# Kernel optimization log

Measured on AMD Instinct MI355X. Metric: run time of the kernel, lower is better.

The kernel has to match this reference:

```python
import jax, jax.numpy as jnp
import numpy as np

B, D, H, Z, E = 65536, 128, 256, 128, 16  # batch, input, hidden, hyper, embedding


def setup_inputs() -> dict:
    key = jax.random.key(0)
    ks = jax.random.split(key, 20)
    s = 0.02  # small weight scale for numerical sanity
    return {
        "x": jax.random.normal(ks[0], (B, D), jnp.float32),
        "h0": jax.random.normal(ks[1], (B, H), jnp.float32),
        "c0": jax.random.normal(ks[2], (B, H), jnp.float32),
        "hhat0": jax.random.normal(ks[3], (B, Z), jnp.float32),
        "chat0": jax.random.normal(ks[4], (B, Z), jnp.float32),
        "hweight": jax.random.normal(ks[5], (Z + H + D, 4 * Z), jnp.float32) * s,
        "hbias": jnp.zeros((4 * Z,), jnp.float32),
        "zw_h": jax.random.normal(ks[6], (Z, 4 * E), jnp.float32) * s,
        "zw_x": jax.random.normal(ks[7], (Z, 4 * E), jnp.float32) * s,
        "zw_b": jax.random.normal(ks[8], (Z, 4 * E), jnp.float32) * 0.01,
        "zb_h": jnp.ones((4 * E,), jnp.float32),
        "zb_x": jnp.ones((4 * E,), jnp.float32),
        "dw_h": jnp.full((4, E, H), 0.1 / E, jnp.float32),  # [i,g,f,o] stacked
        "dw_x": jnp.full((4, E, H), 0.1 / E, jnp.float32),
        "dw_b": jax.random.normal(ks[9], (4, E, H), jnp.float32) * s,
        "weight": jax.random.normal(ks[10], (H + D, 4 * H), jnp.float32) * s,
        "bias": jnp.zeros((4 * H,), jnp.float32),
    }


def reference(x, h0, c0, hhat0, chat0, hweight, hbias, zw_h, zw_x, zw_b,
              zb_h, zb_x, dw_h, dw_x, dw_b, weight, bias):
    sig, tanh = jax.nn.sigmoid, jnp.tanh
    b = x.shape[0]
    # hyper LSTM cell
    gh = jnp.concatenate([hhat0, h0, x], axis=1) @ hweight + hbias  # [B, 4Z]
    i_h, g_h, f_h, o_h = jnp.split(gh, 4, axis=1)
    chat1 = sig(f_h) * chat0 + sig(i_h) * tanh(g_h)
    hhat1 = sig(o_h) * tanh(chat1)
    # embedding projections z (chunk order i,g,f,o -> reshape to [B,4,E])
    z_h = (hhat1 @ zw_h + zb_h).reshape(b, 4, E)
    z_x = (hhat1 @ zw_x + zb_x).reshape(b, 4, E)
    z_b = (hhat1 @ zw_b).reshape(b, 4, E)
    # d scaling vectors, [B,4,H] -> [B,4H]
    d_yh = jnp.einsum('bke,keh->bkh', z_h, dw_h).reshape(b, 4 * H)
    d_yx = jnp.einsum('bke,keh->bkh', z_x, dw_x).reshape(b, 4 * H)
    d_yb = jnp.einsum('bke,keh->bkh', z_b, dw_b).reshape(b, 4 * H)
    # main LSTM gates, hyper-modulated
    g = jnp.concatenate([h0, x], axis=1) @ weight * d_yh * d_yx + d_yb + bias
    i_g, g_g, f_g, o_g = jnp.split(g, 4, axis=1)
    c1 = sig(f_g) * c0 + sig(i_g) * tanh(g_g)
    h1 = sig(o_g) * tanh(c1)
    return (h1, c1, hhat1, chat1)
```

## Files before the change

kernel.cpp:

```cpp
#include <hip/hip_runtime.h>


typedef unsigned short u16;
typedef __attribute__((ext_vector_type(8))) short bf16x8;
typedef __attribute__((ext_vector_type(4))) float f32x4;

#define BATCH 65536

__device__ __forceinline__ u16 f2b(float f) {
  unsigned u = __float_as_uint(f);
  u += 0x7fffu + ((u >> 16) & 1u);
  return (u16)(u >> 16);
}
__device__ __forceinline__ unsigned pk2(float a, float b) {
  return (unsigned)f2b(a) | ((unsigned)f2b(b) << 16);
}
__device__ __forceinline__ float upk_lo(unsigned u) { return __uint_as_float(u << 16); }
__device__ __forceinline__ float upk_hi(unsigned u) { return __uint_as_float(u & 0xffff0000u); }
__device__ __forceinline__ float sigf(float x) { return 1.0f / (1.0f + __expf(-x)); }
__device__ __forceinline__ float tanhfast(float x) {
  float xc = fminf(fmaxf(x, -15.f), 15.f);
  float e = __expf(2.f * xc);
  return (e - 1.f) / (e + 1.f);
}
__device__ __forceinline__ int swz(int r, int c) { return r * 64 + (c ^ ((r & 7) << 3)); }

#define VM_BAR(N) do { \
  asm volatile("s_waitcnt vmcnt(" #N ")" ::: "memory"); \
  __builtin_amdgcn_s_barrier(); \
  __builtin_amdgcn_sched_barrier(0); } while (0)

__device__ __forceinline__ void gl_lds16(const u16* g, u16* l) {
  __builtin_amdgcn_global_load_lds(
      (const __attribute__((address_space(1))) void*)g,
      (__attribute__((address_space(3))) void*)l, 16, 0, 0);
}
__device__ __forceinline__ void stageA(const u16* base, int ldk, u16* lA, int t) {
  const int r = t >> 3, q = t & 7, wid = t >> 6;
  const int qs = (q ^ (r & 7)) << 3;
  gl_lds16(base + (size_t)r * ldk + qs, lA + wid * 512);
  gl_lds16(base + (size_t)(r + 32) * ldk + qs, lA + 2048 + wid * 512);
}

__global__ __launch_bounds__(256) void hlstm_pre(
    const float* __restrict__ hhat0, const float* __restrict__ h0,
    const float* __restrict__ x, u16* __restrict__ abuf,
    const float* __restrict__ hweight, const float* __restrict__ hbias,
    const float* __restrict__ zw_h, const float* __restrict__ zw_x, const float* __restrict__ zw_b,
    const float* __restrict__ zb_h, const float* __restrict__ zb_x,
    const float* __restrict__ dw_h, const float* __restrict__ dw_x, const float* __restrict__ dw_b,
    const float* __restrict__ weight, const float* __restrict__ bias,
    u16* __restrict__ hw_fr, float* __restrict__ hbias_r,
    u16* __restrict__ w_fr,  float* __restrict__ bias_r,
    u16* __restrict__ whp_fr, u16* __restrict__ wxp_fr, u16* __restrict__ wbp_fr,
    float* __restrict__ bhp_r, float* __restrict__ bxp_r)
{
  if (blockIdx.x < 4096) {
    const size_t stride = (size_t)4096 * 256;
    for (size_t i = (size_t)blockIdx.x * 256 + threadIdx.x;
         i < (size_t)BATCH * 64; i += stride) {
      const size_t b = i >> 6; const int c = (int)(i & 63);
      const float* src;
      if (c < 16)      src = hhat0 + b * 128 + c * 8;
      else if (c < 48) src = h0 + b * 256 + (size_t)(c - 16) * 8;
      else             src = x + b * 128 + (size_t)(c - 48) * 8;
      float4 v0 = ((const float4*)src)[0];
      float4 v1 = ((const float4*)src)[1];
      alignas(16) u16 o[8] = {f2b(v0.x), f2b(v0.y), f2b(v0.z), f2b(v0.w),
                              f2b(v1.x), f2b(v1.y), f2b(v1.z), f2b(v1.w)};
      *(uint4*)(abuf + i * 8) = *(const uint4*)o;
    }
    return;
  }
  const int tid = (blockIdx.x - 4096) * 256 + threadIdx.x;
  const int nt  = 512 * 256;

  for (int i = tid; i < 16 * 16384; i += nt) {
    int tile = i >> 14, r = i & 16383;
    int wc = r >> 12, h = (r >> 11) & 1, g = (r >> 9) & 3;
    int lane = (r >> 3) & 63, j = r & 7;
    int hb = tile >> 3, s = tile & 7;
    int k = s * 64 + h * 32 + (lane >> 4) * 8 + j;
    int col = g * 128 + hb * 64 + wc * 16 + (lane & 15);
    hw_fr[i] = f2b(hweight[k * 512 + col]);
  }
  for (int i = tid; i < 24 * 16384; i += nt) {
    int tile = i >> 14, r = i & 16383;
    int wc = r >> 12, h = (r >> 11) & 1, g = (r >> 9) & 3;
    int lane = (r >> 3) & 63, j = r & 7;
    int hb = tile / 6, s = tile % 6;
    int k = s * 64 + h * 32 + (lane >> 4) * 8 + j;
    int col = g * 256 + hb * 64 + wc * 16 + (lane & 15);
    w_fr[i] = f2b(weight[k * 1024 + col]);
  }
  for (int i = tid; i < 3 * 8 * 16384; i += nt) {
    int mat = i / (8 * 16384), rem = i % (8 * 16384);
    int tile = rem >> 14, r = rem & 16383;
    int wc = r >> 12, h = (r >> 11) & 1, g = (r >> 9) & 3;
    int lane = (r >> 3) & 63, j = r & 7;
    int hb = tile >> 1, s = tile & 1;
    int k = s * 64 + h * 32 + (lane >> 4) * 8 + j;
    int colh = hb * 64 + wc * 16 + (lane & 15);
    const float* zw = (mat == 0) ? zw_h : (mat == 1) ? zw_x : zw_b;
    const float* dw = (mat == 0) ? dw_h : (mat == 1) ? dw_x : dw_b;
    float sv = 0.f;
#pragma unroll
    for (int e = 0; e < 16; ++e)
      sv += zw[k * 64 + g * 16 + e] * dw[g * 4096 + e * 256 + colh];
    u16* dst = (mat == 0) ? whp_fr : (mat == 1) ? wxp_fr : wbp_fr;
    dst[rem] = f2b(sv);
  }
  for (int i = tid; i < 1024; i += nt) {
    int hb = i >> 8, g = (i >> 6) & 3, hh = i & 63;
    int h = hb * 64 + hh;
    float sh = 0.f, sx = 0.f;
#pragma unroll
    for (int e = 0; e < 16; ++e) {
      sh += zb_h[g * 16 + e] * dw_h[g * 4096 + e * 256 + h];
      sx += zb_x[g * 16 + e] * dw_x[g * 4096 + e * 256 + h];
    }
    bhp_r[i] = sh; bxp_r[i] = sx;
    bias_r[i] = bias[g * 256 + h];
  }
  for (int i = tid; i < 512; i += nt) {
    int gate = (i >> 6) & 3, hb = i >> 8, hh = i & 63;
    hbias_r[i] = hbias[gate * 128 + hb * 64 + hh];
  }
}

__global__ __launch_bounds__(256, 3) void hlstm_k1(
    const u16* __restrict__ abuf, const float* __restrict__ chat0,
    const u16* __restrict__ hw_fr, const float* __restrict__ hbias_r,
    float* __restrict__ d_out, u16* __restrict__ hbuf)
{
  __shared__ alignas(16) u16 lA[3][64 * 64];
  const int f = blockIdx.x;
  const int xcd = f & 7, s2 = f >> 3;
  const int rb = xcd * 128 + (s2 >> 1), hb = s2 & 1;
  const int t = threadIdx.x;
  const int lane = t & 63, wc = t >> 6;
  const int lr = lane & 15, kg = lane >> 4;

  f32x4 acc[4][4];
  const f32x4 zzero = {0.f, 0.f, 0.f, 0.f};
#pragma unroll
  for (int mf = 0; mf < 4; ++mf)
#pragma unroll
    for (int g = 0; g < 4; ++g) acc[mf][g] = zzero;

  const u16* arow = abuf + (size_t)rb * 64 * 512;

  bf16x8 breg[8];
  auto loadB = [&](const u16* bt) {
#pragma unroll
    for (int h = 0; h < 2; ++h)
#pragma unroll
      for (int g = 0; g < 4; ++g)
        breg[h * 4 + g] = *(const bf16x8*)&bt[((wc * 2 + h) * 4 + g) * 512 + lane * 8];
  };
  auto sweep = [&](f32x4 (&ac)[4][4], const u16* cA) {
#pragma unroll
    for (int h = 0; h < 2; ++h)
#pragma unroll
      for (int mf = 0; mf < 4; ++mf) {
        bf16x8 afr = *(const bf16x8*)&cA[swz(mf * 16 + lr, h * 32 + kg * 8)];
#pragma unroll
        for (int g = 0; g < 4; ++g)
          ac[mf][g] = __builtin_amdgcn_mfma_f32_16x16x32_bf16(afr, breg[h * 4 + g], ac[mf][g], 0, 0, 0);
      }
  };

  stageA(arow + 0 * 64, 512, lA[0], t);
  stageA(arow + 1 * 64, 512, lA[1], t);
  loadB(hw_fr + (size_t)(hb * 8 + 0) * 16384);
  VM_BAR(8);

#pragma unroll
  for (int ks = 0; ks < 8; ++ks) {
    if (ks < 6) stageA(arow + (ks + 2) * 64, 512, lA[(ks + 2) % 3], t);
    sweep(acc, lA[ks % 3]);
    if (ks < 7) loadB(hw_fr + (size_t)(hb * 8 + ks + 1) * 16384);
    if (ks < 6)       VM_BAR(10);
    else if (ks == 6) VM_BAR(8);
  }

  float hb4[4];
#pragma unroll
  for (int g = 0; g < 4; ++g) hb4[g] = hbias_r[hb * 256 + g * 64 + wc * 16 + lr];
  const int zc = hb * 64 + wc * 16 + lr;
  float* out_hh = d_out + (size_t)BATCH * 512;
  float* out_ch = d_out + (size_t)BATCH * 640;
#pragma unroll
  for (int mf = 0; mf < 4; ++mf)
#pragma unroll
    for (int r = 0; r < 4; ++r) {
      const int row = rb * 64 + mf * 16 + kg * 4 + r;
      const float gi = acc[mf][0][r] + hb4[0];
      const float gg = acc[mf][1][r] + hb4[1];
      const float gf = acc[mf][2][r] + hb4[2];
      const float go = acc[mf][3][r] + hb4[3];
      const float c0v = chat0[(size_t)row * 128 + zc];
      const float c1v = sigf(gf) * c0v + sigf(gi) * tanhfast(gg);
      const float h1v = sigf(go) * tanhfast(c1v);
      out_hh[(size_t)row * 128 + zc] = h1v;
      out_ch[(size_t)row * 128 + zc] = c1v;
      hbuf[(size_t)row * 128 + zc] = f2b(h1v);
    }
}

__global__ __launch_bounds__(256, 2) void hlstm_k2(
    const u16* __restrict__ abuf, const u16* __restrict__ hbuf,
    const float* __restrict__ c0,
    const u16* __restrict__ w_fr, const float* __restrict__ bias_r,
    const u16* __restrict__ whp_fr, const u16* __restrict__ wxp_fr, const u16* __restrict__ wbp_fr,
    const float* __restrict__ bhp_r, const float* __restrict__ bxp_r,
    float* __restrict__ d_out)
{
  __shared__ alignas(16) u16 lA[3][64 * 64];
  const int f = blockIdx.x;
  const int xcd = f & 7, s4 = f >> 3;
  const int rb = xcd * 128 + (s4 >> 2), hb = s4 & 3;
  const int t = threadIdx.x;
  const int lane = t & 63, wc = t >> 6;
  const int lr = lane & 15, kg = lane >> 4;

  const u16* amain = abuf + (size_t)rb * 64 * 512 + 128;
  const u16* ahyp  = hbuf + (size_t)rb * 64 * 128;

  auto aptr = [&](int s) -> const u16* {
    if (s >= 4 && s < 10) return amain + (s - 4) * 64;
    return ahyp + (s & 1) * 64;
  };
  auto aldk = [&](int s) -> int { return (s >= 4 && s < 10) ? 512 : 128; };
  auto bptr = [&](int s) -> const u16* {
    if (s < 2)  return whp_fr + (size_t)(hb * 2 + s) * 16384;
    if (s < 4)  return wxp_fr + (size_t)(hb * 2 + s - 2) * 16384;
    if (s < 10) return w_fr  + (size_t)(hb * 6 + s - 4) * 16384;
    return wbp_fr + (size_t)(hb * 2 + s - 10) * 16384;
  };

  f32x4 acc[4][4];
  const f32x4 zzero = {0.f, 0.f, 0.f, 0.f};
#pragma unroll
  for (int mf = 0; mf < 4; ++mf)
#pragma unroll
    for (int g = 0; g < 4; ++g) acc[mf][g] = zzero;

  unsigned dsc[4][4][2];

  bf16x8 breg[8];
  auto loadB = [&](const u16* bt) {
#pragma unroll
    for (int h = 0; h < 2; ++h)
#pragma unroll
      for (int g = 0; g < 4; ++g)
        breg[h * 4 + g] = *(const bf16x8*)&bt[((wc * 2 + h) * 4 + g) * 512 + lane * 8];
  };
  auto sweep = [&](f32x4 (&ac)[4][4], const u16* cA) {
#pragma unroll
    for (int h = 0; h < 2; ++h)
#pragma unroll
      for (int mf = 0; mf < 4; ++mf) {
        bf16x8 afr = *(const bf16x8*)&cA[swz(mf * 16 + lr, h * 32 + kg * 8)];
#pragma unroll
        for (int g = 0; g < 4; ++g)
          ac[mf][g] = __builtin_amdgcn_mfma_f32_16x16x32_bf16(afr, breg[h * 4 + g], ac[mf][g], 0, 0, 0);
      }
  };

  stageA(aptr(0), aldk(0), lA[0], t);
  stageA(aptr(1), aldk(1), lA[1], t);
  loadB(bptr(0));
  VM_BAR(8);

#pragma unroll
  for (int s = 0; s < 12; ++s) {
    if (s < 10) stageA(aptr(s + 2), aldk(s + 2), lA[(s + 2) % 3], t);
    if (s == 2 || s == 4) {
#pragma unroll
      for (int mf = 0; mf < 4; ++mf)
#pragma unroll
        for (int g = 0; g < 4; ++g) acc[mf][g] = zzero;
    }
    sweep(acc, lA[s % 3]);
    if (s < 11) loadB(bptr(s + 1));
    if (s == 1) {
      float bh4[4];
#pragma unroll
      for (int g = 0; g < 4; ++g) bh4[g] = bhp_r[hb * 256 + g * 64 + wc * 16 + lr];
#pragma unroll
      for (int mf = 0; mf < 4; ++mf)
#pragma unroll
        for (int g = 0; g < 4; ++g) {
          dsc[mf][g][0] = pk2(acc[mf][g][0] + bh4[g], acc[mf][g][1] + bh4[g]);
          dsc[mf][g][1] = pk2(acc[mf][g][2] + bh4[g], acc[mf][g][3] + bh4[g]);
        }
    } else if (s == 3) {
      float bx4[4];
#pragma unroll
      for (int g = 0; g < 4; ++g) bx4[g] = bxp_r[hb * 256 + g * 64 + wc * 16 + lr];
#pragma unroll
      for (int mf = 0; mf < 4; ++mf)
#pragma unroll
        for (int g = 0; g < 4; ++g) {
          float d0 = upk_lo(dsc[mf][g][0]) * (acc[mf][g][0] + bx4[g]);
          float d1 = upk_hi(dsc[mf][g][0]) * (acc[mf][g][1] + bx4[g]);
          float d2 = upk_lo(dsc[mf][g][1]) * (acc[mf][g][2] + bx4[g]);
          float d3 = upk_hi(dsc[mf][g][1]) * (acc[mf][g][3] + bx4[g]);
          dsc[mf][g][0] = pk2(d0, d1);
          dsc[mf][g][1] = pk2(d2, d3);
        }
    } else if (s == 9) {
#pragma unroll
      for (int mf = 0; mf < 4; ++mf)
#pragma unroll
        for (int g = 0; g < 4; ++g) {
          acc[mf][g][0] *= upk_lo(dsc[mf][g][0]);
          acc[mf][g][1] *= upk_hi(dsc[mf][g][0]);
          acc[mf][g][2] *= upk_lo(dsc[mf][g][1]);
          acc[mf][g][3] *= upk_hi(dsc[mf][g][1]);
        }
    }
    if (s < 10)       VM_BAR(10);
    else if (s == 10) VM_BAR(8);
  }

  const int hcol = hb * 64 + wc * 16 + lr;
  float b4[4];
#pragma unroll
  for (int g = 0; g < 4; ++g) b4[g] = bias_r[hb * 256 + g * 64 + wc * 16 + lr];
  float* out_c1 = d_out + (size_t)BATCH * 256;
#pragma unroll
  for (int mf = 0; mf < 4; ++mf)
#pragma unroll
    for (int r = 0; r < 4; ++r) {
      const int row = rb * 64 + mf * 16 + kg * 4 + r;
      const float gi = acc[mf][0][r] + b4[0];
      const float gg = acc[mf][1][r] + b4[1];
      const float gf = acc[mf][2][r] + b4[2];
      const float go = acc[mf][3][r] + b4[3];
      const float c0v = c0[(size_t)row * 256 + hcol];
      const float c1v = sigf(gf) * c0v + sigf(gi) * tanhfast(gg);
      const float h1v = sigf(go) * tanhfast(c1v);
      d_out[(size_t)row * 256 + hcol]  = h1v;
      out_c1[(size_t)row * 256 + hcol] = c1v;
    }
}

extern "C" void kernel_launch(void* const* d_in, const int* in_sizes, int n_in,
                              void* d_out, int out_size, void* d_ws, size_t ws_size,
                              hipStream_t stream)
{
  (void)in_sizes; (void)n_in; (void)out_size; (void)ws_size;
  const float* x       = (const float*)d_in[0];
  const float* h0      = (const float*)d_in[1];
  const float* c0      = (const float*)d_in[2];
  const float* hhat0   = (const float*)d_in[3];
  const float* chat0   = (const float*)d_in[4];
  const float* hweight = (const float*)d_in[5];
  const float* hbias   = (const float*)d_in[6];
  const float* zw_h    = (const float*)d_in[7];
  const float* zw_x    = (const float*)d_in[8];
  const float* zw_b    = (const float*)d_in[9];
  const float* zb_h    = (const float*)d_in[10];
  const float* zb_x    = (const float*)d_in[11];
  const float* dw_h    = (const float*)d_in[12];
  const float* dw_x    = (const float*)d_in[13];
  const float* dw_b    = (const float*)d_in[14];
  const float* weight  = (const float*)d_in[15];
  const float* bias    = (const float*)d_in[16];

  char* wsb = (char*)d_ws;
  u16*   abuf    = (u16*)(wsb + 0);
  u16*   hbuf    = (u16*)(wsb + 67108864);
  u16*   hw_fr   = (u16*)(wsb + 83886080);
  u16*   w_fr    = (u16*)(wsb + 84410368);
  u16*   whp_fr  = (u16*)(wsb + 85196800);
  u16*   wxp_fr  = (u16*)(wsb + 85458944);
  u16*   wbp_fr  = (u16*)(wsb + 85721088);
  float* hbias_r = (float*)(wsb + 85983232);
  float* bias_r  = (float*)(wsb + 85985280);
  float* bhp_r   = (float*)(wsb + 85989376);
  float* bxp_r   = (float*)(wsb + 85993472);

  hlstm_pre<<<dim3(4608), dim3(256), 0, stream>>>(
      hhat0, h0, x, abuf,
      hweight, hbias, zw_h, zw_x, zw_b, zb_h, zb_x, dw_h, dw_x, dw_b, weight, bias,
      hw_fr, hbias_r, w_fr, bias_r, whp_fr, wxp_fr, wbp_fr, bhp_r, bxp_r);

  hlstm_k1<<<dim3(2048), dim3(256), 0, stream>>>(
      abuf, chat0, hw_fr, hbias_r, (float*)d_out, hbuf);

  hlstm_k2<<<dim3(4096), dim3(256), 0, stream>>>(
      abuf, hbuf, c0, w_fr, bias_r, whp_fr, wxp_fr, wbp_fr, bhp_r, bxp_r, (float*)d_out);
}
```

Baseline: 273.6 us.

## Pre-pack activations in MFMA fragment order and load A directly to registers

The pre-pass now writes the bf16 activation matrix in MFMA fragment order, so each lane's 16-byte A fragment is contiguous. Both GEMM kernels drop the LDS triple-buffer staging with global_load_lds and barriers, and instead double-buffer A and B fragments in registers by K-half. The aim is to remove the LDS round trip and block-wide synchronisation. The trade-off is that each of the four waves now reads the same A tile from global/L2 separately, which multiplies A traffic, and it raises register pressure.

New measurement: 391.3 us. 43.0% more time.

```diff
diff --git a/kernel.cpp b/kernel.cpp
--- a/kernel.cpp
+++ b/kernel.cpp
@@ -23,28 +23,10 @@
   float e = __expf(2.f * xc);
   return (e - 1.f) / (e + 1.f);
 }
-__device__ __forceinline__ int swz(int r, int c) { return r * 64 + (c ^ ((r & 7) << 3)); }
-
-#define VM_BAR(N) do { \
-  asm volatile("s_waitcnt vmcnt(" #N ")" ::: "memory"); \
-  __builtin_amdgcn_s_barrier(); \
-  __builtin_amdgcn_sched_barrier(0); } while (0)
-
-__device__ __forceinline__ void gl_lds16(const u16* g, u16* l) {
-  __builtin_amdgcn_global_load_lds(
-      (const __attribute__((address_space(1))) void*)g,
-      (__attribute__((address_space(3))) void*)l, 16, 0, 0);
-}
-__device__ __forceinline__ void stageA(const u16* base, int ldk, u16* lA, int t) {
-  const int r = t >> 3, q = t & 7, wid = t >> 6;
-  const int qs = (q ^ (r & 7)) << 3;
-  gl_lds16(base + (size_t)r * ldk + qs, lA + wid * 512);
-  gl_lds16(base + (size_t)(r + 32) * ldk + qs, lA + 2048 + wid * 512);
-}
 
 __global__ __launch_bounds__(256) void hlstm_pre(
     const float* __restrict__ hhat0, const float* __restrict__ h0,
-    const float* __restrict__ x, u16* __restrict__ abuf,
+    const float* __restrict__ x, u16* __restrict__ abuf_fr,
     const float* __restrict__ hweight, const float* __restrict__ hbias,
     const float* __restrict__ zw_h, const float* __restrict__ zw_x, const float* __restrict__ zw_b,
     const float* __restrict__ zb_h, const float* __restrict__ zb_x,
@@ -58,17 +40,23 @@
   if (blockIdx.x < 4096) {
     const size_t stride = (size_t)4096 * 256;
     for (size_t i = (size_t)blockIdx.x * 256 + threadIdx.x;
-         i < (size_t)BATCH * 64; i += stride) {
-      const size_t b = i >> 6; const int c = (int)(i & 63);
+         i < (size_t)4194304; i += stride) {
+      const int lane = (int)(i & 63);
+      const int h    = (int)((i >> 6) & 1);
+      const int mf   = (int)((i >> 7) & 3);
+      const int kc   = (int)((i >> 9) & 7);
+      const int rb   = (int)(i >> 12);
+      const int row = rb * 64 + mf * 16 + (lane & 15);
+      const int col = kc * 64 + h * 32 + (lane >> 4) * 8;
       const float* src;
-      if (c < 16)      src = hhat0 + b * 128 + c * 8;
-      else if (c < 48) src = h0 + b * 256 + (size_t)(c - 16) * 8;
-      else             src = x + b * 128 + (size_t)(c - 48) * 8;
+      if (col < 128)      src = hhat0 + (size_t)row * 128 + col;
+      else if (col < 384) src = h0 + (size_t)row * 256 + (col - 128);
+      else                src = x + (size_t)row * 128 + (col - 384);
       float4 v0 = ((const float4*)src)[0];
       float4 v1 = ((const float4*)src)[1];
       alignas(16) u16 o[8] = {f2b(v0.x), f2b(v0.y), f2b(v0.z), f2b(v0.w),
                               f2b(v1.x), f2b(v1.y), f2b(v1.z), f2b(v1.w)};
-      *(uint4*)(abuf + i * 8) = *(const uint4*)o;
+      *(uint4*)(abuf_fr + i * 8) = *(const uint4*)o;
     }
     return;
   }
@@ -129,11 +117,10 @@
 }
 
 __global__ __launch_bounds__(256, 3) void hlstm_k1(
-    const u16* __restrict__ abuf, const float* __restrict__ chat0,
+    const u16* __restrict__ abuf_fr, const float* __restrict__ chat0,
     const u16* __restrict__ hw_fr, const float* __restrict__ hbias_r,
     float* __restrict__ d_out, u16* __restrict__ hbuf)
 {
-  __shared__ alignas(16) u16 lA[3][64 * 64];
   const int f = blockIdx.x;
   const int xcd = f & 7, s2 = f >> 3;
   const int rb = xcd * 128 + (s2 >> 1), hb = s2 & 1;
@@ -148,40 +135,34 @@
 #pragma unroll
     for (int g = 0; g < 4; ++g) acc[mf][g] = zzero;
 
-  const u16* arow = abuf + (size_t)rb * 64 * 512;
-
-  bf16x8 breg[8];
-  auto loadB = [&](const u16* bt) {
-#pragma unroll
-    for (int h = 0; h < 2; ++h)
+  bf16x8 A0[4], A1[4], B0[4], B1[4];
+  auto loadA = [&](bf16x8 (&Ar)[4], int kc, int h) {
+#pragma unroll
+    for (int mf = 0; mf < 4; ++mf)
+      Ar[mf] = *(const bf16x8*)&abuf_fr[((((size_t)rb * 8 + kc) * 4 + mf) * 2 + h) * 512 + lane * 8];
+  };
+  auto loadBh = [&](bf16x8 (&Br)[4], const u16* bt, int h) {
+#pragma unroll
+    for (int g = 0; g < 4; ++g)
+      Br[g] = *(const bf16x8*)&bt[((wc * 2 + h) * 4 + g) * 512 + lane * 8];
+  };
+  auto half = [&](const bf16x8 (&Ar)[4], const bf16x8 (&Br)[4]) {
+#pragma unroll
+    for (int mf = 0; mf < 4; ++mf)
 #pragma unroll
       for (int g = 0; g < 4; ++g)
-        breg[h * 4 + g] = *(const bf16x8*)&bt[((wc * 2 + h) * 4 + g) * 512 + lane * 8];
-  };
-  auto sweep = [&](f32x4 (&ac)[4][4], const u16* cA) {
-#pragma unroll
-    for (int h = 0; h < 2; ++h)
-#pragma unroll
-      for (int mf = 0; mf < 4; ++mf) {
-        bf16x8 afr = *(const bf16x8*)&cA[swz(mf * 16 + lr, h * 32 + kg * 8)];
-#pragma unroll
-        for (int g = 0; g < 4; ++g)
-          ac[mf][g] = __builtin_amdgcn_mfma_f32_16x16x32_bf16(afr, breg[h * 4 + g], ac[mf][g], 0, 0, 0);
-      }
-  };
-
-  stageA(arow + 0 * 64, 512, lA[0], t);
-  stageA(arow + 1 * 64, 512, lA[1], t);
-  loadB(hw_fr + (size_t)(hb * 8 + 0) * 16384);
-  VM_BAR(8);
+        acc[mf][g] = __builtin_amdgcn_mfma_f32_16x16x32_bf16(Ar[mf], Br[g], acc[mf][g], 0, 0, 0);
+  };
+
+  loadA(A0, 0, 0); loadBh(B0, hw_fr + (size_t)(hb * 8) * 16384, 0);
+  loadA(A1, 0, 1); loadBh(B1, hw_fr + (size_t)(hb * 8) * 16384, 1);
 
 #pragma unroll
   for (int ks = 0; ks < 8; ++ks) {
-    if (ks < 6) stageA(arow + (ks + 2) * 64, 512, lA[(ks + 2) % 3], t);
-    sweep(acc, lA[ks % 3]);
-    if (ks < 7) loadB(hw_fr + (size_t)(hb * 8 + ks + 1) * 16384);
-    if (ks < 6)       VM_BAR(10);
-    else if (ks == 6) VM_BAR(8);
+    half(A0, B0);
+    if (ks < 7) { loadA(A0, ks + 1, 0); loadBh(B0, hw_fr + (size_t)(hb * 8 + ks + 1) * 16384, 0); }
+    half(A1, B1);
+    if (ks < 7) { loadA(A1, ks + 1, 1); loadBh(B1, hw_fr + (size_t)(hb * 8 + ks + 1) * 16384, 1); }
   }
 
   float hb4[4];
@@ -209,14 +190,13 @@
 }
 
 __global__ __launch_bounds__(256, 2) void hlstm_k2(
-    const u16* __restrict__ abuf, const u16* __restrict__ hbuf,
+    const u16* __restrict__ abuf_fr, const u16* __restrict__ hbuf,
     const float* __restrict__ c0,
     const u16* __restrict__ w_fr, const float* __restrict__ bias_r,
     const u16* __restrict__ whp_fr, const u16* __restrict__ wxp_fr, const u16* __restrict__ wbp_fr,
     const float* __restrict__ bhp_r, const float* __restrict__ bxp_r,
     float* __restrict__ d_out)
 {
-  __shared__ alignas(16) u16 lA[3][64 * 64];
   const int f = blockIdx.x;
   const int xcd = f & 7, s4 = f >> 3;
   const int rb = xcd * 128 + (s4 >> 2), hb = s4 & 3;
@@ -224,14 +204,6 @@
   const int lane = t & 63, wc = t >> 6;
   const int lr = lane & 15, kg = lane >> 4;
 
-  const u16* amain = abuf + (size_t)rb * 64 * 512 + 128;
-  const u16* ahyp  = hbuf + (size_t)rb * 64 * 128;
-
-  auto aptr = [&](int s) -> const u16* {
-    if (s >= 4 && s < 10) return amain + (s - 4) * 64;
-    return ahyp + (s & 1) * 64;
-  };
-  auto aldk = [&](int s) -> int { return (s >= 4 && s < 10) ? 512 : 128; };
   auto bptr = [&](int s) -> const u16* {
     if (s < 2)  return whp_fr + (size_t)(hb * 2 + s) * 16384;
     if (s < 4)  return wxp_fr + (size_t)(hb * 2 + s - 2) * 16384;
@@ -248,42 +220,49 @@
 
   unsigned dsc[4][4][2];
 
-  bf16x8 breg[8];
-  auto loadB = [&](const u16* bt) {
-#pragma unroll
-    for (int h = 0; h < 2; ++h)
+  bf16x8 A0[4], A1[4], B0[4], B1[4];
+  auto loadA = [&](bf16x8 (&Ar)[4], int s, int h) {
+    if (s >= 4 && s < 10) {
+      const int kc = s - 2;
+#pragma unroll
+      for (int mf = 0; mf < 4; ++mf)
+        Ar[mf] = *(const bf16x8*)&abuf_fr[((((size_t)rb * 8 + kc) * 4 + mf) * 2 + h) * 512 + lane * 8];
+    } else {
+      const int c = s & 1;
+#pragma unroll
+      for (int mf = 0; mf < 4; ++mf)
+        Ar[mf] = *(const bf16x8*)&hbuf[(size_t)(rb * 64 + mf * 16 + lr) * 128 + c * 64 + h * 32 + kg * 8];
+    }
+  };
+  auto loadBh = [&](bf16x8 (&Br)[4], const u16* bt, int h) {
+#pragma unroll
+    for (int g = 0; g < 4; ++g)
+      Br[g] = *(const bf16x8*)&bt[((wc * 2 + h) * 4 + g) * 512 + lane * 8];
+  };
+  auto half = [&](const bf16x8 (&Ar)[4], const bf16x8 (&Br)[4]) {
+#pragma unroll
+    for (int mf = 0; mf < 4; ++mf)
 #pragma unroll
       for (int g = 0; g < 4; ++g)
-        breg[h * 4 + g] = *(const bf16x8*)&bt[((wc * 2 + h) * 4 + g) * 512 + lane * 8];
-  };
-  auto sweep = [&](f32x4 (&ac)[4][4], const u16* cA) {
-#pragma unroll
-    for (int h = 0; h < 2; ++h)
-#pragma unroll
-      for (int mf = 0; mf < 4; ++mf) {
-        bf16x8 afr = *(const bf16x8*)&cA[swz(mf * 16 + lr, h * 32 + kg * 8)];
-#pragma unroll
-        for (int g = 0; g < 4; ++g)
-          ac[mf][g] = __builtin_amdgcn_mfma_f32_16x16x32_bf16(afr, breg[h * 4 + g], ac[mf][g], 0, 0, 0);
-      }
-  };
-
-  stageA(aptr(0), aldk(0), lA[0], t);
-  stageA(aptr(1), aldk(1), lA[1], t);
-  loadB(bptr(0));
-  VM_BAR(8);
+        acc[mf][g] = __builtin_amdgcn_mfma_f32_16x16x32_bf16(Ar[mf], Br[g], acc[mf][g], 0, 0, 0);
+  };
+
+  loadA(A0, 0, 0); loadBh(B0, bptr(0), 0);
+  loadA(A1, 0, 1); loadBh(B1, bptr(0), 1);
 
 #pragma unroll
   for (int s = 0; s < 12; ++s) {
-    if (s < 10) stageA(aptr(s + 2), aldk(s + 2), lA[(s + 2) % 3], t);
     if (s == 2 || s == 4) {
 #pragma unroll
       for (int mf = 0; mf < 4; ++mf)
 #pragma unroll
         for (int g = 0; g < 4; ++g) acc[mf][g] = zzero;
     }
-    sweep(acc, lA[s % 3]);
-    if (s < 11) loadB(bptr(s + 1));
+    half(A0, B0);
+    if (s < 11) { loadA(A0, s + 1, 0); loadBh(B0, bptr(s + 1), 0); }
+    half(A1, B1);
+    if (s < 11) { loadA(A1, s + 1, 1); loadBh(B1, bptr(s + 1), 1); }
+
     if (s == 1) {
       float bh4[4];
 #pragma unroll
@@ -321,8 +300,6 @@
           acc[mf][g][3] *= upk_hi(dsc[mf][g][1]);
         }
     }
-    if (s < 10)       VM_BAR(10);
-    else if (s == 10) VM_BAR(8);
   }
 
   const int hcol = hb * 64 + wc * 16 + lr;
@@ -371,7 +348,7 @@
   const float* bias    = (const float*)d_in[16];
 
   char* wsb = (char*)d_ws;
-  u16*   abuf    = (u16*)(wsb + 0);
+  u16*   abuf_fr = (u16*)(wsb + 0);
   u16*   hbuf    = (u16*)(wsb + 67108864);
   u16*   hw_fr   = (u16*)(wsb + 83886080);
   u16*   w_fr    = (u16*)(wsb + 84410368);
@@ -384,13 +361,13 @@
   float* bxp_r   = (float*)(wsb + 85993472);
 
   hlstm_pre<<<dim3(4608), dim3(256), 0, stream>>>(
-      hhat0, h0, x, abuf,
+      hhat0, h0, x, abuf_fr,
       hweight, hbias, zw_h, zw_x, zw_b, zb_h, zb_x, dw_h, dw_x, dw_b, weight, bias,
       hw_fr, hbias_r, w_fr, bias_r, whp_fr, wxp_fr, wbp_fr, bhp_r, bxp_r);
 
   hlstm_k1<<<dim3(2048), dim3(256), 0, stream>>>(
-      abuf, chat0, hw_fr, hbias_r, (float*)d_out, hbuf);
+      abuf_fr, chat0, hw_fr, hbias_r, (float*)d_out, hbuf);
 
   hlstm_k2<<<dim3(4096), dim3(256), 0, stream>>>(
-      abuf, hbuf, c0, w_fr, bias_r, whp_fr, wxp_fr, wbp_fr, bhp_r, bxp_r, (float*)d_out);
-}
+      abuf_fr, hbuf, c0, w_fr, bias_r, whp_fr, wxp_fr, wbp_fr, bhp_r, bxp_r, (float*)d_out);
+}
```

## Split GEMM blocks into single-wave blocks that each stage their own A tile

Applied to the files above, without the earlier changes.

Both GEMM kernels move from 256-thread blocks, where four waves share a cooperatively staged A tile, to 64-thread single-wave blocks. Each wave now stages the full 64x64 A tile itself through a double buffer and uses only a per-wave vmcnt wait instead of a block barrier. MFMA sweeps are also wrapped in s_setprio. This removes the block-wide barrier stalls, but each A tile is now loaded four times over (once per wave), which raises global/L2 traffic and LDS footprint per computed column.

Result: slower. 294.8 us (+7.7%).

```diff
diff --git a/kernel.cpp b/kernel.cpp
--- a/kernel.cpp
+++ b/kernel.cpp
@@ -25,9 +25,8 @@
 }
 __device__ __forceinline__ int swz(int r, int c) { return r * 64 + (c ^ ((r & 7) << 3)); }
 
-#define VM_BAR(N) do { \
-  asm volatile("s_waitcnt vmcnt(" #N ")" ::: "memory"); \
-  __builtin_amdgcn_s_barrier(); \
+#define WAVE_FENCE8() do { \
+  asm volatile("s_waitcnt vmcnt(8)" ::: "memory"); \
   __builtin_amdgcn_sched_barrier(0); } while (0)
 
 __device__ __forceinline__ void gl_lds16(const u16* g, u16* l) {
@@ -35,11 +34,12 @@
       (const __attribute__((address_space(1))) void*)g,
       (__attribute__((address_space(3))) void*)l, 16, 0, 0);
 }
-__device__ __forceinline__ void stageA(const u16* base, int ldk, u16* lA, int t) {
-  const int r = t >> 3, q = t & 7, wid = t >> 6;
-  const int qs = (q ^ (r & 7)) << 3;
-  gl_lds16(base + (size_t)r * ldk + qs, lA + wid * 512);
-  gl_lds16(base + (size_t)(r + 32) * ldk + qs, lA + 2048 + wid * 512);
+__device__ __forceinline__ void stageA1(const u16* base, int ldk, u16* dst, int lane) {
+  const int rsub = lane >> 3;
+  const int qs = ((lane & 7) ^ rsub) << 3;
+#pragma unroll
+  for (int c = 0; c < 8; ++c)
+    gl_lds16(base + (size_t)(c * 8 + rsub) * ldk + qs, dst + c * 512);
 }
 
 __global__ __launch_bounds__(256) void hlstm_pre(
@@ -128,17 +128,17 @@
   }
 }
 
-__global__ __launch_bounds__(256, 3) void hlstm_k1(
+__global__ __launch_bounds__(64, 2) void hlstm_k1(
     const u16* __restrict__ abuf, const float* __restrict__ chat0,
     const u16* __restrict__ hw_fr, const float* __restrict__ hbias_r,
     float* __restrict__ d_out, u16* __restrict__ hbuf)
 {
-  __shared__ alignas(16) u16 lA[3][64 * 64];
+  __shared__ alignas(16) u16 lA[2][64 * 64];
   const int f = blockIdx.x;
-  const int xcd = f & 7, s2 = f >> 3;
-  const int rb = xcd * 128 + (s2 >> 1), hb = s2 & 1;
-  const int t = threadIdx.x;
-  const int lane = t & 63, wc = t >> 6;
+  const int xcd = f & 7, u = f >> 3;
+  const int rb = xcd * 128 + (u >> 3);
+  const int sub = u & 7, hb = sub >> 2, wc = sub & 3;
+  const int lane = threadIdx.x;
   const int lr = lane & 15, kg = lane >> 4;
 
   f32x4 acc[4][4];
@@ -158,7 +158,8 @@
       for (int g = 0; g < 4; ++g)
         breg[h * 4 + g] = *(const bf16x8*)&bt[((wc * 2 + h) * 4 + g) * 512 + lane * 8];
   };
-  auto sweep = [&](f32x4 (&ac)[4][4], const u16* cA) {
+  auto sweep = [&](const u16* cA) {
+    __builtin_amdgcn_s_setprio(1);
 #pragma unroll
     for (int h = 0; h < 2; ++h)
 #pragma unroll
@@ -166,22 +167,20 @@
         bf16x8 afr = *(const bf16x8*)&cA[swz(mf * 16 + lr, h * 32 + kg * 8)];
 #pragma unroll
         for (int g = 0; g < 4; ++g)
-          ac[mf][g] = __builtin_amdgcn_mfma_f32_16x16x32_bf16(afr, breg[h * 4 + g], ac[mf][g], 0, 0, 0);
+          acc[mf][g] = __builtin_amdgcn_mfma_f32_16x16x32_bf16(afr, breg[h * 4 + g], acc[mf][g], 0, 0, 0);
       }
-  };
-
-  stageA(arow + 0 * 64, 512, lA[0], t);
-  stageA(arow + 1 * 64, 512, lA[1], t);
-  loadB(hw_fr + (size_t)(hb * 8 + 0) * 16384);
-  VM_BAR(8);
+    __builtin_amdgcn_s_setprio(0);
+  };
+
+  stageA1(arow, 512, lA[0], lane);
+  loadB(hw_fr + (size_t)(hb * 8) * 16384);
 
 #pragma unroll
   for (int ks = 0; ks < 8; ++ks) {
-    if (ks < 6) stageA(arow + (ks + 2) * 64, 512, lA[(ks + 2) % 3], t);
-    sweep(acc, lA[ks % 3]);
+    WAVE_FENCE8();
+    if (ks < 7) stageA1(arow + (ks + 1) * 64, 512, lA[(ks + 1) & 1], lane);
+    sweep(lA[ks & 1]);
     if (ks < 7) loadB(hw_fr + (size_t)(hb * 8 + ks + 1) * 16384);
-    if (ks < 6)       VM_BAR(10);
-    else if (ks == 6) VM_BAR(8);
   }
 
   float hb4[4];
@@ -208,7 +207,7 @@
     }
 }
 
-__global__ __launch_bounds__(256, 2) void hlstm_k2(
+__global__ __launch_bounds__(64, 2) void hlstm_k2(
     const u16* __restrict__ abuf, const u16* __restrict__ hbuf,
     const float* __restrict__ c0,
     const u16* __restrict__ w_fr, const float* __restrict__ bias_r,
@@ -216,12 +215,12 @@
     const float* __restrict__ bhp_r, const float* __restrict__ bxp_r,
     float* __restrict__ d_out)
 {
-  __shared__ alignas(16) u16 lA[3][64 * 64];
+  __shared__ alignas(16) u16 lA[2][64 * 64];
   const int f = blockIdx.x;
-  const int xcd = f & 7, s4 = f >> 3;
-  const int rb = xcd * 128 + (s4 >> 2), hb = s4 & 3;
-  const int t = threadIdx.x;
-  const int lane = t & 63, wc = t >> 6;
+  const int xcd = f & 7, u = f >> 3;
+  const int rb = xcd * 128 + (u >> 4);
+  const int sub = u & 15, hb = sub >> 2, wc = sub & 3;
+  const int lane = threadIdx.x;
   const int lr = lane & 15, kg = lane >> 4;
 
   const u16* amain = abuf + (size_t)rb * 64 * 512 + 128;
@@ -256,7 +255,8 @@
       for (int g = 0; g < 4; ++g)
         breg[h * 4 + g] = *(const bf16x8*)&bt[((wc * 2 + h) * 4 + g) * 512 + lane * 8];
   };
-  auto sweep = [&](f32x4 (&ac)[4][4], const u16* cA) {
+  auto sweep = [&](const u16* cA) {
+    __builtin_amdgcn_s_setprio(1);
 #pragma unroll
     for (int h = 0; h < 2; ++h)
 #pragma unroll
@@ -264,26 +264,27 @@
         bf16x8 afr = *(const bf16x8*)&cA[swz(mf * 16 + lr, h * 32 + kg * 8)];
 #pragma unroll
         for (int g = 0; g < 4; ++g)
-          ac[mf][g] = __builtin_amdgcn_mfma_f32_16x16x32_bf16(afr, breg[h * 4 + g], ac[mf][g], 0, 0, 0);
+          acc[mf][g] = __builtin_amdgcn_mfma_f32_16x16x32_bf16(afr, breg[h * 4 + g], acc[mf][g], 0, 0, 0);
       }
-  };
-
-  stageA(aptr(0), aldk(0), lA[0], t);
-  stageA(aptr(1), aldk(1), lA[1], t);
+    __builtin_amdgcn_s_setprio(0);
+  };
+
+  stageA1(aptr(0), aldk(0), lA[0], lane);
   loadB(bptr(0));
-  VM_BAR(8);
 
 #pragma unroll
   for (int s = 0; s < 12; ++s) {
-    if (s < 10) stageA(aptr(s + 2), aldk(s + 2), lA[(s + 2) % 3], t);
+    WAVE_FENCE8();
     if (s == 2 || s == 4) {
 #pragma unroll
       for (int mf = 0; mf < 4; ++mf)
 #pragma unroll
         for (int g = 0; g < 4; ++g) acc[mf][g] = zzero;
     }
-    sweep(acc, lA[s % 3]);
+    if (s < 11) stageA1(aptr(s + 1), aldk(s + 1), lA[(s + 1) & 1], lane);
+    sweep(lA[s & 1]);
     if (s < 11) loadB(bptr(s + 1));
+
     if (s == 1) {
       float bh4[4];
 #pragma unroll
@@ -321,8 +322,6 @@
           acc[mf][g][3] *= upk_hi(dsc[mf][g][1]);
         }
     }
-    if (s < 10)       VM_BAR(10);
-    else if (s == 10) VM_BAR(8);
   }
 
   const int hcol = hb * 64 + wc * 16 + lr;
@@ -388,9 +387,9 @@
       hweight, hbias, zw_h, zw_x, zw_b, zb_h, zb_x, dw_h, dw_x, dw_b, weight, bias,
       hw_fr, hbias_r, w_fr, bias_r, whp_fr, wxp_fr, wbp_fr, bhp_r, bxp_r);
 
-  hlstm_k1<<<dim3(2048), dim3(256), 0, stream>>>(
+  hlstm_k1<<<dim3(8192), dim3(64), 0, stream>>>(
       abuf, chat0, hw_fr, hbias_r, (float*)d_out, hbuf);
 
-  hlstm_k2<<<dim3(4096), dim3(256), 0, stream>>>(
+  hlstm_k2<<<dim3(16384), dim3(64), 0, stream>>>(
       abuf, hbuf, c0, w_fr, bias_r, whp_fr, wxp_fr, wbp_fr, bhp_r, bxp_r, (float*)d_out);
 }
```

## Retile GEMM kernels to 128-row blocks with 2x2 warps and LDS-staged B

Applied to the files above, without the earlier changes.

Both GEMM kernels now use 128-row by 32-column tiles split over a 2x2 wave grid, instead of 64-row tiles where each wave covered its own column slice. The weight fragments are repacked into 32-column tiles and loaded into LDS through global_load_lds, where they were previously read straight from global memory into registers. The pipeline moves from triple-buffered A with partial vmcnt waits to double-buffered A and B with full waits. The aim is more reuse of A and B per block; in exchange each block uses more LDS, occupancy drops to 2 blocks per CU, and load latency is less well hidden.

Result: no change. 278.5 us (+1.8%).

```diff
diff --git a/kernel.cpp b/kernel.cpp
--- a/kernel.cpp
+++ b/kernel.cpp
@@ -25,10 +25,11 @@
 }
 __device__ __forceinline__ int swz(int r, int c) { return r * 64 + (c ^ ((r & 7) << 3)); }
 
-#define VM_BAR(N) do { \
-  asm volatile("s_waitcnt vmcnt(" #N ")" ::: "memory"); \
-  __builtin_amdgcn_s_barrier(); \
-  __builtin_amdgcn_sched_barrier(0); } while (0)
+__device__ __forceinline__ void wait0_bar() {
+  asm volatile("s_waitcnt vmcnt(0)" ::: "memory");
+  __builtin_amdgcn_s_barrier();
+  __builtin_amdgcn_sched_barrier(0);
+}
 
 __device__ __forceinline__ void gl_lds16(const u16* g, u16* l) {
   __builtin_amdgcn_global_load_lds(
@@ -40,6 +41,12 @@
   const int qs = (q ^ (r & 7)) << 3;
   gl_lds16(base + (size_t)r * ldk + qs, lA + wid * 512);
   gl_lds16(base + (size_t)(r + 32) * ldk + qs, lA + 2048 + wid * 512);
+}
+__device__ __forceinline__ void stageB16(const u16* tile, u16* lB, int t) {
+  const int wid = t >> 6;
+#pragma unroll
+  for (int i = 0; i < 4; ++i)
+    gl_lds16(tile + ((size_t)i * 256 + t) * 8, lB + i * 2048 + wid * 512);
 }
 
 __global__ __launch_bounds__(256) void hlstm_pre(
@@ -75,32 +82,33 @@
   const int tid = (blockIdx.x - 4096) * 256 + threadIdx.x;
   const int nt  = 512 * 256;
 
-  for (int i = tid; i < 16 * 16384; i += nt) {
-    int tile = i >> 14, r = i & 16383;
-    int wc = r >> 12, h = (r >> 11) & 1, g = (r >> 9) & 3;
+  for (int i = tid; i < 32 * 8192; i += nt) {
+    int tile = i >> 13, r = i & 8191;
+    int wn = r >> 12, h = (r >> 11) & 1, g = (r >> 9) & 3;
     int lane = (r >> 3) & 63, j = r & 7;
-    int hb = tile >> 3, s = tile & 7;
+    int hb = tile >> 4, hh32 = (tile >> 3) & 1, s = tile & 7;
     int k = s * 64 + h * 32 + (lane >> 4) * 8 + j;
-    int col = g * 128 + hb * 64 + wc * 16 + (lane & 15);
+    int col = g * 128 + hb * 64 + hh32 * 32 + wn * 16 + (lane & 15);
     hw_fr[i] = f2b(hweight[k * 512 + col]);
   }
-  for (int i = tid; i < 24 * 16384; i += nt) {
-    int tile = i >> 14, r = i & 16383;
-    int wc = r >> 12, h = (r >> 11) & 1, g = (r >> 9) & 3;
+  for (int i = tid; i < 48 * 8192; i += nt) {
+    int tile = i >> 13, r = i & 8191;
+    int wn = r >> 12, h = (r >> 11) & 1, g = (r >> 9) & 3;
     int lane = (r >> 3) & 63, j = r & 7;
-    int hb = tile / 6, s = tile % 6;
+    int hb = tile / 12, rem = tile % 12;
+    int hh32 = rem / 6, s = rem % 6;
     int k = s * 64 + h * 32 + (lane >> 4) * 8 + j;
-    int col = g * 256 + hb * 64 + wc * 16 + (lane & 15);
+    int col = g * 256 + hb * 64 + hh32 * 32 + wn * 16 + (lane & 15);
     w_fr[i] = f2b(weight[k * 1024 + col]);
   }
-  for (int i = tid; i < 3 * 8 * 16384; i += nt) {
-    int mat = i / (8 * 16384), rem = i % (8 * 16384);
-    int tile = rem >> 14, r = rem & 16383;
-    int wc = r >> 12, h = (r >> 11) & 1, g = (r >> 9) & 3;
+  for (int i = tid; i < 3 * 16 * 8192; i += nt) {
+    int mat = i / 131072, rem2 = i % 131072;
+    int tile = rem2 >> 13, r = rem2 & 8191;
+    int wn = r >> 12, h = (r >> 11) & 1, g = (r >> 9) & 3;
     int lane = (r >> 3) & 63, j = r & 7;
-    int hb = tile >> 1, s = tile & 1;
+    int hb = tile >> 2, hh32 = (tile >> 1) & 1, s = tile & 1;
     int k = s * 64 + h * 32 + (lane >> 4) * 8 + j;
-    int colh = hb * 64 + wc * 16 + (lane & 15);
+    int colh = hb * 64 + hh32 * 32 + wn * 16 + (lane & 15);
     const float* zw = (mat == 0) ? zw_h : (mat == 1) ? zw_x : zw_b;
     const float* dw = (mat == 0) ? dw_h : (mat == 1) ? dw_x : dw_b;
     float sv = 0.f;
@@ -108,7 +116,7 @@
     for (int e = 0; e < 16; ++e)
       sv += zw[k * 64 + g * 16 + e] * dw[g * 4096 + e * 256 + colh];
     u16* dst = (mat == 0) ? whp_fr : (mat == 1) ? wxp_fr : wbp_fr;
-    dst[rem] = f2b(sv);
+    dst[rem2] = f2b(sv);
   }
   for (int i = tid; i < 1024; i += nt) {
     int hb = i >> 8, g = (i >> 6) & 3, hh = i & 63;
@@ -128,17 +136,20 @@
   }
 }
 
-__global__ __launch_bounds__(256, 3) void hlstm_k1(
+__global__ __launch_bounds__(256, 2) void hlstm_k1(
     const u16* __restrict__ abuf, const float* __restrict__ chat0,
     const u16* __restrict__ hw_fr, const float* __restrict__ hbias_r,
     float* __restrict__ d_out, u16* __restrict__ hbuf)
 {
-  __shared__ alignas(16) u16 lA[3][64 * 64];
+  __shared__ alignas(16) u16 lA[2][8192];
+  __shared__ alignas(16) u16 lB[2][8192];
   const int f = blockIdx.x;
-  const int xcd = f & 7, s2 = f >> 3;
-  const int rb = xcd * 128 + (s2 >> 1), hb = s2 & 1;
+  const int xcd = f & 7, u = f >> 3;
+  const int rb = xcd * 64 + (u >> 2);
+  const int sub = u & 3, hb = sub >> 1, hh32 = sub & 1;
   const int t = threadIdx.x;
-  const int lane = t & 63, wc = t >> 6;
+  const int lane = t & 63, w = t >> 6;
+  const int wm = w >> 1, wn = w & 1;
   const int lr = lane & 15, kg = lane >> 4;
 
   f32x4 acc[4][4];
@@ -148,53 +159,54 @@
 #pragma unroll
     for (int g = 0; g < 4; ++g) acc[mf][g] = zzero;
 
-  const u16* arow = abuf + (size_t)rb * 64 * 512;
-
-  bf16x8 breg[8];
-  auto loadB = [&](const u16* bt) {
-#pragma unroll
-    for (int h = 0; h < 2; ++h)
+  const u16* arow = abuf + (size_t)rb * 128 * 512;
+  auto btile = [&](int s) -> const u16* {
+    return hw_fr + (size_t)((hb * 2 + hh32) * 8 + s) * 8192;
+  };
+  auto stage = [&](int s, int buf) {
+    stageA(arow + s * 64, 512, lA[buf], t);
+    stageA(arow + s * 64 + (size_t)64 * 512, 512, lA[buf] + 4096, t);
+    stageB16(btile(s), lB[buf], t);
+  };
+  auto sweep = [&](const u16* cA, const u16* cB) {
+#pragma unroll
+    for (int h = 0; h < 2; ++h) {
+      bf16x8 bfr[4];
 #pragma unroll
       for (int g = 0; g < 4; ++g)
-        breg[h * 4 + g] = *(const bf16x8*)&bt[((wc * 2 + h) * 4 + g) * 512 + lane * 8];
-  };
-  auto sweep = [&](f32x4 (&ac)[4][4], const u16* cA) {
-#pragma unroll
-    for (int h = 0; h < 2; ++h)
+        bfr[g] = *(const bf16x8*)&cB[wn * 4096 + (h * 4 + g) * 512 + lane * 8];
 #pragma unroll
       for (int mf = 0; mf < 4; ++mf) {
-        bf16x8 afr = *(const bf16x8*)&cA[swz(mf * 16 + lr, h * 32 + kg * 8)];
+        bf16x8 afr = *(const bf16x8*)&cA[swz(wm * 64 + mf * 16 + lr, h * 32 + kg * 8)];
 #pragma unroll
         for (int g = 0; g < 4; ++g)
-          ac[mf][g] = __builtin_amdgcn_mfma_f32_16x16x32_bf16(afr, breg[h * 4 + g], ac[mf][g], 0, 0, 0);
+          acc[mf][g] = __builtin_amdgcn_mfma_f32_16x16x32_bf16(afr, bfr[g], acc[mf][g], 0, 0, 0);
       }
-  };
-
-  stageA(arow + 0 * 64, 512, lA[0], t);
-  stageA(arow + 1 * 64, 512, lA[1], t);
-  loadB(hw_fr + (size_t)(hb * 8 + 0) * 16384);
-  VM_BAR(8);
-
+    }
+  };
+
+  stage(0, 0);
+  wait0_bar();
 #pragma unroll
   for (int ks = 0; ks < 8; ++ks) {
-    if (ks < 6) stageA(arow + (ks + 2) * 64, 512, lA[(ks + 2) % 3], t);
-    sweep(acc, lA[ks % 3]);
-    if (ks < 7) loadB(hw_fr + (size_t)(hb * 8 + ks + 1) * 16384);
-    if (ks < 6)       VM_BAR(10);
-    else if (ks == 6) VM_BAR(8);
+    const int cur = ks & 1;
+    if (ks < 7) stage(ks + 1, cur ^ 1);
+    sweep(lA[cur], lB[cur]);
+    if (ks < 7) wait0_bar();
   }
 
   float hb4[4];
 #pragma unroll
-  for (int g = 0; g < 4; ++g) hb4[g] = hbias_r[hb * 256 + g * 64 + wc * 16 + lr];
-  const int zc = hb * 64 + wc * 16 + lr;
+  for (int g = 0; g < 4; ++g)
+    hb4[g] = hbias_r[hb * 256 + g * 64 + hh32 * 32 + wn * 16 + lr];
+  const int zc = hb * 64 + hh32 * 32 + wn * 16 + lr;
   float* out_hh = d_out + (size_t)BATCH * 512;
   float* out_ch = d_out + (size_t)BATCH * 640;
 #pragma unroll
   for (int mf = 0; mf < 4; ++mf)
 #pragma unroll
     for (int r = 0; r < 4; ++r) {
-      const int row = rb * 64 + mf * 16 + kg * 4 + r;
+      const int row = rb * 128 + wm * 64 + mf * 16 + kg * 4 + r;
       const float gi = acc[mf][0][r] + hb4[0];
       const float gg = acc[mf][1][r] + hb4[1];
       const float gf = acc[mf][2][r] + hb4[2];
@@ -216,16 +228,19 @@
     const float* __restrict__ bhp_r, const float* __restrict__ bxp_r,
     float* __restrict__ d_out)
 {
-  __shared__ alignas(16) u16 lA[3][64 * 64];
+  __shared__ alignas(16) u16 lA[2][8192];
+  __shared__ alignas(16) u16 lB[2][8192];
   const int f = blockIdx.x;
-  const int xcd = f & 7, s4 = f >> 3;
-  const int rb = xcd * 128 + (s4 >> 2), hb = s4 & 3;
+  const int xcd = f & 7, u = f >> 3;
+  const int rb = xcd * 64 + (u >> 3);
+  const int sub = u & 7, hb = sub >> 1, hh32 = sub & 1;
   const int t = threadIdx.x;
-  const int lane = t & 63, wc = t >> 6;
+  const int lane = t & 63, w = t >> 6;
+  const int wm = w >> 1, wn = w & 1;
   const int lr = lane & 15, kg = lane >> 4;
 
-  const u16* amain = abuf + (size_t)rb * 64 * 512 + 128;
-  const u16* ahyp  = hbuf + (size_t)rb * 64 * 128;
+  const u16* amain = abuf + (size_t)rb * 128 * 512 + 128;
+  const u16* ahyp  = hbuf + (size_t)rb * 128 * 128;
 
   auto aptr = [&](int s) -> const u16* {
     if (s >= 4 && s < 10) return amain + (s - 4) * 64;
@@ -233,10 +248,11 @@
   };
   auto aldk = [&](int s) -> int { return (s >= 4 && s < 10) ? 512 : 128; };
   auto bptr = [&](int s) -> const u16* {
-    if (s < 2)  return whp_fr + (size_t)(hb * 2 + s) * 16384;
-    if (s < 4)  return wxp_fr + (size_t)(hb * 2 + s - 2) * 16384;
-    if (s < 10) return w_fr  + (size_t)(hb * 6 + s - 4) * 16384;
-    return wbp_fr + (size_t)(hb * 2 + s - 10) * 16384;
+    const int base = (hb * 2 + hh32);
+    if (s < 2)  return whp_fr + (size_t)(base * 2 + s) * 8192;
+    if (s < 4)  return wxp_fr + (size_t)(base * 2 + s - 2) * 8192;
+    if (s < 10) return w_fr  + (size_t)(base * 6 + s - 4) * 8192;
+    return wbp_fr + (size_t)(base * 2 + s - 10) * 8192;
   };
 
   f32x4 acc[4][4];
@@ -248,46 +264,48 @@
 
   unsigned dsc[4][4][2];
 
-  bf16x8 breg[8];
-  auto loadB = [&](const u16* bt) {
-#pragma unroll
-    for (int h = 0; h < 2; ++h)
+  auto stage = [&](int s, int buf) {
+    const u16* ap = aptr(s); const int ldk = aldk(s);
+    stageA(ap, ldk, lA[buf], t);
+    stageA(ap + (size_t)64 * ldk, ldk, lA[buf] + 4096, t);
+    stageB16(bptr(s), lB[buf], t);
+  };
+  auto sweep = [&](const u16* cA, const u16* cB) {
+#pragma unroll
+    for (int h = 0; h < 2; ++h) {
+      bf16x8 bfr[4];
 #pragma unroll
       for (int g = 0; g < 4; ++g)
-        breg[h * 4 + g] = *(const bf16x8*)&bt[((wc * 2 + h) * 4 + g) * 512 + lane * 8];
-  };
-  auto sweep = [&](f32x4 (&ac)[4][4], const u16* cA) {
-#pragma unroll
-    for (int h = 0; h < 2; ++h)
+        bfr[g] = *(const bf16x8*)&cB[wn * 4096 + (h * 4 + g) * 512 + lane * 8];
 #pragma unroll
       for (int mf = 0; mf < 4; ++mf) {
-        bf16x8 afr = *(const bf16x8*)&cA[swz(mf * 16 + lr, h * 32 + kg * 8)];
+        bf16x8 afr = *(const bf16x8*)&cA[swz(wm * 64 + mf * 16 + lr, h * 32 + kg * 8)];
 #pragma unroll
         for (int g = 0; g < 4; ++g)
-          ac[mf][g] = __builtin_amdgcn_mfma_f32_16x16x32_bf16(afr, breg[h * 4 + g], ac[mf][g], 0, 0, 0);
+          acc[mf][g] = __builtin_amdgcn_mfma_f32_16x16x32_bf16(afr, bfr[g], acc[mf][g], 0, 0, 0);
       }
-  };
-
-  stageA(aptr(0), aldk(0), lA[0], t);
-  stageA(aptr(1), aldk(1), lA[1], t);
-  loadB(bptr(0));
-  VM_BAR(8);
-
+    }
+  };
+
+  stage(0, 0);
+  wait0_bar();
 #pragma unroll
   for (int s = 0; s < 12; ++s) {
-    if (s < 10) stageA(aptr(s + 2), aldk(s + 2), lA[(s + 2) % 3], t);
+    const int cur = s & 1;
+    if (s < 11) stage(s + 1, cur ^ 1);
     if (s == 2 || s == 4) {
 #pragma unroll
       for (int mf = 0; mf < 4; ++mf)
 #pragma unroll
         for (int g = 0; g < 4; ++g) acc[mf][g] = zzero;
     }
-    sweep(acc, lA[s % 3]);
-    if (s < 11) loadB(bptr(s + 1));
+    sweep(lA[cur], lB[cur]);
+
     if (s == 1) {
       float bh4[4];
 #pragma unroll
-      for (int g = 0; g < 4; ++g) bh4[g] = bhp_r[hb * 256 + g * 64 + wc * 16 + lr];
+      for (int g = 0; g < 4; ++g)
+        bh4[g] = bhp_r[hb * 256 + g * 64 + hh32 * 32 + wn * 16 + lr];
 #pragma unroll
       for (int mf = 0; mf < 4; ++mf)
 #pragma unroll
@@ -298,7 +316,8 @@
     } else if (s == 3) {
       float bx4[4];
 #pragma unroll
-      for (int g = 0; g < 4; ++g) bx4[g] = bxp_r[hb * 256 + g * 64 + wc * 16 + lr];
+      for (int g = 0; g < 4; ++g)
+        bx4[g] = bxp_r[hb * 256 + g * 64 + hh32 * 32 + wn * 16 + lr];
 #pragma unroll
       for (int mf = 0; mf < 4; ++mf)
 #pragma unroll
@@ -321,20 +340,20 @@
           acc[mf][g][3] *= upk_hi(dsc[mf][g][1]);
         }
     }
-    if (s < 10)       VM_BAR(10);
-    else if (s == 10) VM_BAR(8);
-  }
-
-  const int hcol = hb * 64 + wc * 16 + lr;
+    if (s < 11) wait0_bar();
+  }
+
+  const int hcol = hb * 64 + hh32 * 32 + wn * 16 + lr;
   float b4[4];
 #pragma unroll
-  for (int g = 0; g < 4; ++g) b4[g] = bias_r[hb * 256 + g * 64 + wc * 16 + lr];
+  for (int g = 0; g < 4; ++g)
+    b4[g] = bias_r[hb * 256 + g * 64 + hh32 * 32 + wn * 16 + lr];
   float* out_c1 = d_out + (size_t)BATCH * 256;
 #pragma unroll
   for (int mf = 0; mf < 4; ++mf)
 #pragma unroll
     for (int r = 0; r < 4; ++r) {
-      const int row = rb * 64 + mf * 16 + kg * 4 + r;
+      const int row = rb * 128 + wm * 64 + mf * 16 + kg * 4 + r;
       const float gi = acc[mf][0][r] + b4[0];
       const float gg = acc[mf][1][r] + b4[1];
       const float gf = acc[mf][2][r] + b4[2];
```
